# Optimization experiments

Hardware: AMD Instinct MI355X
Metric: run time of the kernel (lower is better)

## Reference

```python
import jax, jax.numpy as jnp
import numpy as np

N, MAX_NB, H, L, V, B, M = 16384, 15, 512, 128, 1024, 256, 65536


def setup_inputs() -> dict:
    key = jax.random.key(0)
    ks = jax.random.split(key, 32)
    s = 0.02  # param init scale
    inp = {
        'x_ids': jax.random.randint(ks[0], (N,), 0, V, dtype=jnp.int32),
        'contexts': jax.random.randint(ks[1], (N,), 0, B, dtype=jnp.int32),
        'nei_idx': jax.random.randint(ks[2], (N, MAX_NB), 0, M, dtype=jnp.int32),
        'nei_mask': jax.random.randint(ks[3], (N, MAX_NB), 0, 2, dtype=jnp.int32),
        'o_idx': jax.random.randint(ks[4], (N, MAX_NB), 0, M, dtype=jnp.int32),
        'o_mask': jax.random.randint(ks[5], (N, MAX_NB), 0, 2, dtype=jnp.int32),
        'H_msg': jax.random.normal(ks[6], (M, H), jnp.float32),
        'x_tree_vecs': jax.random.normal(ks[7], (B, L), jnp.float32),
        'embedding': jax.random.normal(ks[8], (V, H), jnp.float32) * s,
        'Wz_w': jax.random.normal(ks[9], (H, 2 * H), jnp.float32) * s,
        'Wz_b': jnp.zeros((H,), jnp.float32),
        'Wr_w': jax.random.normal(ks[10], (H, H), jnp.float32) * s,
        'Wr_b': jnp.zeros((H,), jnp.float32),
        'Ur_w': jax.random.normal(ks[11], (H, H), jnp.float32) * s,
        'Wh_w': jax.random.normal(ks[12], (H, 2 * H), jnp.float32) * s,
        'Wh_b': jnp.zeros((H,), jnp.float32),
        'W_w': jax.random.normal(ks[13], (H, H + L), jnp.float32) * s,
        'W_b': jnp.zeros((H,), jnp.float32),
        'Wo_w': jax.random.normal(ks[14], (V, H), jnp.float32) * s,
        'Wo_b': jnp.zeros((V,), jnp.float32),
        'Ui_w': jax.random.normal(ks[15], (H, 2 * H), jnp.float32) * s,
        'Ui_b': jnp.zeros((H,), jnp.float32),
        'U_w': jax.random.normal(ks[16], (H, H + L), jnp.float32) * s,
        'U_b': jnp.zeros((H,), jnp.float32),
        'Uo_w': jax.random.normal(ks[17], (1, H), jnp.float32) * s,
        'Uo_b': jnp.zeros((1,), jnp.float32),
    }
    return inp


def _gru(x, h_nei, Wz_w, Wz_b, Wr_w, Wr_b, Ur_w, Wh_w, Wh_b):
    # x: [N,H], h_nei: [N,MAX_NB,H]
    sum_h = h_nei.sum(axis=1)
    z = jax.nn.sigmoid(jnp.concatenate([x, sum_h], axis=1) @ Wz_w.T + Wz_b)
    r1 = (x @ Wr_w.T + Wr_b)[:, None, :]          # [N,1,H]
    r2 = jnp.einsum('nkh,gh->nkg', h_nei, Ur_w)   # U_r(h_nei), no bias
    r = jax.nn.sigmoid(r1 + r2)
    sum_gated = (r * h_nei).sum(axis=1)
    pre_h = jnp.tanh(jnp.concatenate([x, sum_gated], axis=1) @ Wh_w.T + Wh_b)
    return (1.0 - z) * sum_h + z * pre_h


def reference(x_ids, contexts, nei_idx, nei_mask, o_idx, o_mask, H_msg,
              x_tree_vecs, embedding, Wz_w, Wz_b, Wr_w, Wr_b, Ur_w,
              Wh_w, Wh_b, W_w, W_b, Wo_w, Wo_b, Ui_w, Ui_b, U_w, U_b,
              Uo_w, Uo_b):
    x = embedding[x_ids]                                   # [N,H]
    h_nei = H_msg[nei_idx] * nei_mask[..., None].astype(H_msg.dtype)  # [N,NB,H]
    o_nei = H_msg[o_idx] * o_mask[..., None].astype(H_msg.dtype)
    new_h = _gru(x, h_nei, Wz_w, Wz_b, Wr_w, Wr_b, Ur_w, Wh_w, Wh_b)
    cur_o = o_nei.sum(axis=1)                              # [N,H]
    ctx = x_tree_vecs[contexts]                            # [N,L]
    # word prediction: aggregate(new_h, contexts, x_tree_vecs, 'word')
    w_hid = jax.nn.relu(jnp.concatenate([new_h, ctx], axis=1) @ W_w.T + W_b)
    word_scores = w_hid @ Wo_w.T + Wo_b                    # [N,V]
    # stop prediction: U_i(cat(x, cur_o)) -> aggregate(..., 'stop')
    stop_h = jax.nn.relu(jnp.concatenate([x, cur_o], axis=1) @ Ui_w.T + Ui_b)
    s_hid = jax.nn.relu(jnp.concatenate([stop_h, ctx], axis=1) @ U_w.T + U_b)
    stop_scores = s_hid @ Uo_w.T + Uo_b                    # [N,1]
    return jnp.concatenate([word_scores, stop_scores], axis=1)  # [N,V+1]
```

## Files before the change

kernel.cpp:

```cpp
#include <hip/hip_runtime.h>
#include <hip/hip_bf16.h>

typedef unsigned short u16;
typedef unsigned int u32;
typedef __attribute__((ext_vector_type(8))) short s8v;
typedef __attribute__((ext_vector_type(4))) float f4v;

#define HDIM 512
#define NNODE 16384
#define NB 15

__device__ __forceinline__ u16 f2bu(float x) {
  union { float f; u32 i; } v; v.f = x;
  u32 r = v.i + 0x7FFFu + ((v.i >> 16) & 1u);
  return (u16)(r >> 16);
}
__device__ __forceinline__ float bu2f(u16 u) {
  union { u32 i; float f; } v; v.i = ((u32)u) << 16;
  return v.f;
}
__device__ __forceinline__ u32 pk(float a, float b) {
  return (u32)f2bu(a) | ((u32)f2bu(b) << 16);
}
__device__ __forceinline__ float sigm(float x) {
  return __builtin_amdgcn_rcpf(1.f + __expf(-x));
}
__device__ __forceinline__ void gl16(const void* g, void* l) {
  __builtin_amdgcn_global_load_lds(
      (const __attribute__((address_space(1))) u32*)g,
      (__attribute__((address_space(3))) u32*)l, 16, 0, 0);
}

__global__ __launch_bounds__(256) void k_cvt_all(
    const float* Wz_w, const float* Wr_w, const float* Wh_w, const float* Ui_w,
    const float* Ur_w, const float* W_w, const float* U_w, const float* Wo_w,
    const float* emb, const float* xtree,
    const float* Wz_b, const float* Wr_b, const float* Wh_b, const float* Ui_b,
    const float* W_b, const float* U_b,
    u16* wcat, u16* wz_h, u16* wh_h, u16* ui_h, u16* ur, u16* w_n, u16* u_n,
    u16* ccat, u16* wo, u16* emb_bf, u16* xt_bf, float* ebias, float* cbias) {
  int seg = blockIdx.y;
  const float* src = nullptr; u16* dst = nullptr;
  const float* fsrc = nullptr; float* fdst = nullptr;
  int R = 0, Cs = 0, c0 = 0, C = 0, fn = 0;
  switch (seg) {
    case 0:  src = Wz_w; dst = wcat;              R = 512;  Cs = 1024; c0 = 0;   C = 512; break;
    case 1:  src = Wr_w; dst = wcat + 512 * 512;  R = 512;  Cs = 512;  c0 = 0;   C = 512; break;
    case 2:  src = Wh_w; dst = wcat + 1024 * 512; R = 512;  Cs = 1024; c0 = 0;   C = 512; break;
    case 3:  src = Ui_w; dst = wcat + 1536 * 512; R = 512;  Cs = 1024; c0 = 0;   C = 512; break;
    case 4:  src = Wz_w; dst = wz_h;              R = 512;  Cs = 1024; c0 = 512; C = 512; break;
    case 5:  src = Wh_w; dst = wh_h;              R = 512;  Cs = 1024; c0 = 512; C = 512; break;
    case 6:  src = Ui_w; dst = ui_h;              R = 512;  Cs = 1024; c0 = 512; C = 512; break;
    case 7:  src = Ur_w; dst = ur;                R = 512;  Cs = 512;  c0 = 0;   C = 512; break;
    case 8:  src = W_w;  dst = w_n;               R = 512;  Cs = 640;  c0 = 0;   C = 512; break;
    case 9:  src = U_w;  dst = u_n;               R = 512;  Cs = 640;  c0 = 0;   C = 512; break;
    case 10: src = W_w;  dst = ccat;              R = 512;  Cs = 640;  c0 = 512; C = 128; break;
    case 11: src = U_w;  dst = ccat + 512 * 128;  R = 512;  Cs = 640;  c0 = 512; C = 128; break;
    case 12: src = Wo_w; dst = wo;                R = 1024; Cs = 512;  c0 = 0;   C = 512; break;
    case 13: src = emb;  dst = emb_bf;            R = 1024; Cs = 512;  c0 = 0;   C = 512; break;
    case 14: src = xtree; dst = xt_bf;            R = 256;  Cs = 128;  c0 = 0;   C = 128; break;
    case 15: fsrc = Wz_b; fdst = ebias;        fn = 512; break;
    case 16: fsrc = Wr_b; fdst = ebias + 512;  fn = 512; break;
    case 17: fsrc = Wh_b; fdst = ebias + 1024; fn = 512; break;
    case 18: fsrc = Ui_b; fdst = ebias + 1536; fn = 512; break;
    case 19: fsrc = W_b;  fdst = cbias;        fn = 512; break;
    case 20: fsrc = U_b;  fdst = cbias + 512;  fn = 512; break;
  }
  int i = blockIdx.x * 256 + threadIdx.x;
  if (fdst) { if (i < fn) fdst[i] = fsrc[i]; return; }
  int e0 = i * 8;
  if (e0 >= R * C) return;
  int r = e0 / C, c = e0 - r * C;
  const float* s = src + (size_t)r * Cs + c0 + c;
  float4 a = *reinterpret_cast<const float4*>(s);
  float4 b = *reinterpret_cast<const float4*>(s + 4);
  uint4 o = {pk(a.x, a.y), pk(a.z, a.w), pk(b.x, b.y), pk(b.z, b.w)};
  *reinterpret_cast<uint4*>(&dst[e0]) = o;
}

__global__ void k_cvt8(const float* __restrict__ src, u16* __restrict__ dst) {
  size_t i = ((size_t)blockIdx.x * 256 + threadIdx.x) * 8;
  float4 a = *reinterpret_cast<const float4*>(src + i);
  float4 b = *reinterpret_cast<const float4*>(src + i + 4);
  uint4 o = {pk(a.x, a.y), pk(a.z, a.w), pk(b.x, b.y), pk(b.z, b.w)};
  *reinterpret_cast<uint4*>(dst + i) = o;
}

struct GP {
  const u16* A; const u16* B; int K;
  const float* gadd; int ldg; const int* gidx;
  const float* bias; const float* zf; const u16* shb;
  float* outf; u16* outh; int ldo;
};

template<int EP>
__device__ __forceinline__ void epi(int row, int col, float v, const GP& g) {
  if constexpr (EP == 0) {
    g.outf[(size_t)row * g.ldo + col] = v + (g.bias ? g.bias[col] : 0.f);
  } else if constexpr (EP == 1) {
    float pre = v + g.gadd[(size_t)g.gidx[row] * g.ldg + col];
    g.outf[(size_t)row * g.ldo + col] = sigm(pre);
  } else if constexpr (EP == 2) {
    float pre = tanhf(v + g.gadd[(size_t)g.gidx[row] * g.ldg + col]);
    float z = g.zf[(size_t)row * HDIM + col];
    float sh = bu2f(g.shb[(size_t)row * HDIM + col]);
    g.outh[(size_t)row * g.ldo + col] = f2bu((1.f - z) * sh + z * pre);
  } else if constexpr (EP == 3) {
    float pre = v + g.gadd[(size_t)g.gidx[row] * g.ldg + col];
    g.outh[(size_t)row * g.ldo + col] = f2bu(pre > 0.f ? pre : 0.f);
  } else {
    g.outh[(size_t)row * g.ldo + col] = f2bu(v);
  }
}

template<int EP>
__device__ void gemm_core(const GP& g, u16* AsB, u16* BsB) {
  const int tid = threadIdx.x, lane = tid & 63, w = tid >> 6;
  const int wm = (w >> 2) * 64, wn = (w & 3) * 32;
  const int n0 = blockIdx.x * 128, m0 = blockIdx.y * 128;
  const int K = g.K;

  const u16* gA[2]; const u16* gB[2]; int ls[2];
#pragma unroll
  for (int i = 0; i < 2; i++) {
    int slot = tid + i * 512;
    int r = slot >> 3, c = (slot & 7) ^ (r & 7);
    gA[i] = g.A + (size_t)(m0 + r) * K + c * 8;
    gB[i] = g.B + (size_t)(n0 + r) * K + c * 8;
    ls[i] = slot * 8;
  }

  f4v acc[4][2];
  f4v z4 = {0.f, 0.f, 0.f, 0.f};
#pragma unroll
  for (int a = 0; a < 4; a++) { acc[a][0] = z4; acc[a][1] = z4; }

  const int T = K >> 6;
#pragma unroll
  for (int i = 0; i < 2; i++) gl16(gA[i], AsB + ls[i]);
#pragma unroll
  for (int i = 0; i < 2; i++) gl16(gB[i], BsB + ls[i]);

  int cur = 0;
  for (int t = 0; t < T; t++) {
    __syncthreads();
    if (t + 1 < T) {
      int k0 = (t + 1) * 64;
      u16* as = AsB + (cur ^ 1) * 8192;
      u16* bs = BsB + (cur ^ 1) * 8192;
#pragma unroll
      for (int i = 0; i < 2; i++) gl16(gA[i] + k0, as + ls[i]);
#pragma unroll
      for (int i = 0; i < 2; i++) gl16(gB[i] + k0, bs + ls[i]);
    }
    const u16* as = AsB + cur * 8192;
    const u16* bs = BsB + cur * 8192;
#pragma unroll
    for (int ks = 0; ks < 2; ks++) {
      s8v af[4], bf[2];
      int cc = ks * 4 + (lane >> 4);
#pragma unroll
      for (int i = 0; i < 4; i++) {
        int R = wm + i * 16 + (lane & 15);
        af[i] = *reinterpret_cast<const s8v*>(&as[R * 64 + (cc ^ (R & 7)) * 8]);
      }
#pragma unroll
      for (int i = 0; i < 2; i++) {
        int C = wn + i * 16 + (lane & 15);
        bf[i] = *reinterpret_cast<const s8v*>(&bs[C * 64 + (cc ^ (C & 7)) * 8]);
      }
#pragma unroll
      for (int mi = 0; mi < 4; mi++)
#pragma unroll
        for (int ni = 0; ni < 2; ni++)
          acc[mi][ni] = __builtin_amdgcn_mfma_f32_16x16x32_bf16(
              af[mi], bf[ni], acc[mi][ni], 0, 0, 0);
    }
    cur ^= 1;
  }
#pragma unroll
  for (int mi = 0; mi < 4; mi++)
#pragma unroll
    for (int ni = 0; ni < 2; ni++)
#pragma unroll
      for (int r = 0; r < 4; r++) {
        int row = m0 + wm + mi * 16 + (lane >> 4) * 4 + r;
        int col = n0 + wn + ni * 16 + (lane & 15);
        epi<EP>(row, col, acc[mi][ni][r], g);
      }
}

template<int EP>
__global__ __launch_bounds__(512, 4) void k_gemm(GP g) {
  __shared__ u16 As[2 * 128 * 64], Bs[2 * 128 * 64];
  gemm_core<EP>(g, As, Bs);
}

template<int EPa, int EPb>
__global__ __launch_bounds__(512, 4) void k_pair(GP a, GP b) {
  __shared__ u16 As[2 * 128 * 64], Bs[2 * 128 * 64];
  if (blockIdx.z == 0) gemm_core<EPa>(a, As, Bs);
  else gemm_core<EPb>(b, As, Bs);
}

__global__ __launch_bounds__(256) void k_gsr(
    const u16* __restrict__ Hb, const u16* __restrict__ R2,
    const float* __restrict__ E_r, int ldg, const int* __restrict__ x_ids,
    const int* __restrict__ nei_idx, const int* __restrict__ nei_mask,
    const int* __restrict__ o_idx, const int* __restrict__ o_mask,
    u16* __restrict__ sum_h_bf, u16* __restrict__ sg_bf,
    u16* __restrict__ cur_o_bf) {
  int n = blockIdx.x;
  int t = threadIdx.x;
  __shared__ int sidx[NB], smsk[NB], soid[NB], somk[NB];
  __shared__ int sx;
  if (t < NB) {
    sidx[t] = nei_idx[(size_t)n * NB + t];
    smsk[t] = nei_mask[(size_t)n * NB + t];
  } else if (t >= 64 && t < 64 + NB) {
    int k = t - 64;
    soid[k] = o_idx[(size_t)n * NB + k];
    somk[k] = o_mask[(size_t)n * NB + k];
  } else if (t == 128) {
    sx = x_ids[n];
  }
  __syncthreads();
  int c = t * 2;
  const float2 e = *reinterpret_cast<const float2*>(E_r + (size_t)sx * ldg + c);
  float s0 = 0.f, s1 = 0.f, g0 = 0.f, g1 = 0.f, o0 = 0.f, o1 = 0.f;
#pragma unroll
  for (int k = 0; k < NB; k++) {
    if (smsk[k]) {
      u32 hv = *reinterpret_cast<const u32*>(Hb + (size_t)sidx[k] * HDIM + c);
      u32 rv = *reinterpret_cast<const u32*>(R2 + (size_t)sidx[k] * HDIM + c);
      float h0 = bu2f((u16)hv), h1 = bu2f((u16)(hv >> 16));
      float r0 = sigm(bu2f((u16)rv) + e.x);
      float r1 = sigm(bu2f((u16)(rv >> 16)) + e.y);
      s0 += h0; s1 += h1;
      g0 += r0 * h0; g1 += r1 * h1;
    }
    if (somk[k]) {
      u32 v = *reinterpret_cast<const u32*>(Hb + (size_t)soid[k] * HDIM + c);
      o0 += bu2f((u16)v); o1 += bu2f((u16)(v >> 16));
    }
  }
  size_t b = (size_t)n * HDIM + c;
  *reinterpret_cast<u32*>(&sum_h_bf[b]) = pk(s0, s1);
  *reinterpret_cast<u32*>(&sg_bf[b]) = pk(g0, g1);
  *reinterpret_cast<u32*>(&cur_o_bf[b]) = pk(o0, o1);
}

__global__ __launch_bounds__(256) void k_stop(
    const u16* __restrict__ shid, const float* __restrict__ Uo_w,
    const float* __restrict__ Uo_b, float* __restrict__ out) {
  int n = blockIdx.x * 4 + (threadIdx.x >> 6);
  int lane = threadIdx.x & 63;
  float s = 0.f;
  for (int j = lane; j < HDIM; j += 64)
    s += bu2f(shid[(size_t)n * HDIM + j]) * Uo_w[j];
#pragma unroll
  for (int off = 32; off; off >>= 1) s += __shfl_xor(s, off, 64);
  if (lane == 0) out[(size_t)n * 1025 + 1024] = s + Uo_b[0];
}

extern "C" void kernel_launch(void* const* d_in, const int* in_sizes, int n_in,
                              void* d_out, int out_size, void* d_ws, size_t ws_size,
                              hipStream_t stream) {
  const int* x_ids = (const int*)d_in[0];
  const int* contexts = (const int*)d_in[1];
  const int* nei_idx = (const int*)d_in[2];
  const int* nei_mask = (const int*)d_in[3];
  const int* o_idx = (const int*)d_in[4];
  const int* o_mask = (const int*)d_in[5];
  const float* H_msg = (const float*)d_in[6];
  const float* xtree = (const float*)d_in[7];
  const float* emb = (const float*)d_in[8];
  const float* Wz_w = (const float*)d_in[9];  const float* Wz_b = (const float*)d_in[10];
  const float* Wr_w = (const float*)d_in[11]; const float* Wr_b = (const float*)d_in[12];
  const float* Ur_w = (const float*)d_in[13];
  const float* Wh_w = (const float*)d_in[14]; const float* Wh_b = (const float*)d_in[15];
  const float* W_w  = (const float*)d_in[16]; const float* W_b  = (const float*)d_in[17];
  const float* Wo_w = (const float*)d_in[18]; const float* Wo_b = (const float*)d_in[19];
  const float* Ui_w = (const float*)d_in[20]; const float* Ui_b = (const float*)d_in[21];
  const float* U_w  = (const float*)d_in[22]; const float* U_b  = (const float*)d_in[23];
  const float* Uo_w = (const float*)d_in[24]; const float* Uo_b = (const float*)d_in[25];
  float* out = (float*)d_out;
  const int M = 65536;

  char* base = (char*)d_ws;
  size_t ofs = 0;
  auto alloc = [&](size_t bytes) -> char* {
    char* p = base + ofs;
    ofs = (ofs + bytes + 255) & ~(size_t)255;
    return p;
  };
  u16* wcat  = (u16*)alloc((size_t)2048 * 512 * 2);
  u16* wz_h  = (u16*)alloc(512 * 512 * 2);
  u16* wh_h  = (u16*)alloc(512 * 512 * 2);
  u16* ui_h  = (u16*)alloc(512 * 512 * 2);
  u16* ur    = (u16*)alloc(512 * 512 * 2);
  u16* w_n   = (u16*)alloc(512 * 512 * 2);
  u16* u_n   = (u16*)alloc(512 * 512 * 2);
  u16* ccat  = (u16*)alloc(1024 * 128 * 2);
  u16* wo    = (u16*)alloc(1024 * 512 * 2);
  u16* emb_bf = (u16*)alloc(1024 * 512 * 2);
  u16* xt_bf  = (u16*)alloc(256 * 128 * 2);
  float* ebias = (float*)alloc(2048 * 4);
  float* cbias = (float*)alloc(1024 * 4);
  float* E_cat = (float*)alloc((size_t)1024 * 2048 * 4);
  float* C_cat = (float*)alloc((size_t)256 * 1024 * 4);
  u16* H_bf = (u16*)alloc((size_t)M * HDIM * 2);
  u16* R2   = (u16*)alloc((size_t)M * HDIM * 2);
  float* z_f = (float*)alloc((size_t)NNODE * HDIM * 4);
  u16* sum_h_bf = (u16*)alloc((size_t)NNODE * HDIM * 2);
  u16* cur_o_bf = (u16*)alloc((size_t)NNODE * HDIM * 2);
  u16* sg_bf    = (u16*)alloc((size_t)NNODE * HDIM * 2);
  u16* newh_bf  = (u16*)alloc((size_t)NNODE * HDIM * 2);
  u16* whid_bf  = (u16*)alloc((size_t)NNODE * HDIM * 2);
  u16* stoph_bf = (u16*)alloc((size_t)NNODE * HDIM * 2);
  u16* shid_bf  = (u16*)alloc((size_t)NNODE * HDIM * 2);

  k_cvt_all<<<dim3(256, 21), dim3(256), 0, stream>>>(
      Wz_w, Wr_w, Wh_w, Ui_w, Ur_w, W_w, U_w, Wo_w, emb, xtree,
      Wz_b, Wr_b, Wh_b, Ui_b, W_b, U_b,
      wcat, wz_h, wh_h, ui_h, ur, w_n, u_n, ccat, wo, emb_bf, xt_bf,
      ebias, cbias);
  k_cvt8<<<dim3(16384), dim3(256), 0, stream>>>(H_msg, H_bf);

  GP ge{emb_bf, wcat, 512, nullptr, 0, nullptr, ebias, nullptr, nullptr,
        E_cat, nullptr, 2048};
  k_gemm<0><<<dim3(16, 8), dim3(512), 0, stream>>>(ge);
  GP gc{xt_bf, ccat, 128, nullptr, 0, nullptr, cbias, nullptr, nullptr,
        C_cat, nullptr, 1024};
  k_gemm<0><<<dim3(8, 2), dim3(512), 0, stream>>>(gc);

  GP gr{H_bf, ur, 512, nullptr, 0, nullptr, nullptr, nullptr, nullptr,
        nullptr, R2, 512};
  k_gemm<4><<<dim3(4, 512), dim3(512), 0, stream>>>(gr);

  k_gsr<<<dim3(NNODE), dim3(256), 0, stream>>>(
      H_bf, R2, E_cat + 512, 2048, x_ids, nei_idx, nei_mask, o_idx, o_mask,
      sum_h_bf, sg_bf, cur_o_bf);

  GP gz{sum_h_bf, wz_h, 512, E_cat, 2048, x_ids, nullptr, nullptr, nullptr,
        z_f, nullptr, 512};
  GP gs{cur_o_bf, ui_h, 512, E_cat + 1536, 2048, x_ids, nullptr, nullptr, nullptr,
        nullptr, stoph_bf, 512};
  k_pair<1, 3><<<dim3(4, 128, 2), dim3(512), 0, stream>>>(gz, gs);

  GP gn{sg_bf, wh_h, 512, E_cat + 1024, 2048, x_ids, nullptr, z_f, sum_h_bf,
        nullptr, newh_bf, 512};
  k_gemm<2><<<dim3(4, 128), dim3(512), 0, stream>>>(gn);

  GP gw{newh_bf, w_n, 512, C_cat, 1024, contexts, nullptr, nullptr, nullptr,
        nullptr, whid_bf, 512};
  GP gu{stoph_bf, u_n, 512, C_cat + 512, 1024, contexts, nullptr, nullptr, nullptr,
        nullptr, shid_bf, 512};
  k_pair<3, 3><<<dim3(4, 128, 2), dim3(512), 0, stream>>>(gw, gu);

  GP gword{whid_bf, wo, 512, nullptr, 0, nullptr, Wo_b, nullptr, nullptr,
           out, nullptr, 1025};
  k_gemm<0><<<dim3(8, 128), dim3(512), 0, stream>>>(gword);

  k_stop<<<dim3(NNODE / 4), dim3(256), 0, stream>>>(shid_bf, Uo_w, Uo_b, out);
}
```

Baseline: 358.0 us.

## Fuse z and candidate GEMMs, interleave H and R2 rows, swizzle tile order

The z-gate GEMM and the candidate-state GEMM now run in one kernel with two accumulator sets. That kernel computes sigmoid, tanh and the GRU blend in its epilogue, so the fp32 z buffer and its round trip through memory go away. H_bf and R2 are stored interleaved in a single [M,1024] buffer, so each gathered neighbor row brings H and R from adjacent memory. GEMM tiles are also remapped with a stride-8 swizzle to change L2 locality across blocks. The costs are higher register pressure in the fused kernel, which has no double buffering, and the stop GEMM now launches alone instead of paired.

Result: faster. 333.0 us (-7.0%).

```diff
diff --git a/kernel.cpp b/kernel.cpp
--- a/kernel.cpp
+++ b/kernel.cpp
@@ -78,18 +78,19 @@
   *reinterpret_cast<uint4*>(&dst[e0]) = o;
 }
 
-__global__ void k_cvt8(const float* __restrict__ src, u16* __restrict__ dst) {
+__global__ void k_cvtH(const float* __restrict__ src, u16* __restrict__ HR) {
   size_t i = ((size_t)blockIdx.x * 256 + threadIdx.x) * 8;
+  size_t m = i >> 9, c = i & 511;
   float4 a = *reinterpret_cast<const float4*>(src + i);
   float4 b = *reinterpret_cast<const float4*>(src + i + 4);
   uint4 o = {pk(a.x, a.y), pk(a.z, a.w), pk(b.x, b.y), pk(b.z, b.w)};
-  *reinterpret_cast<uint4*>(dst + i) = o;
+  *reinterpret_cast<uint4*>(&HR[m * 1024 + c]) = o;
 }
 
 struct GP {
-  const u16* A; const u16* B; int K;
+  const u16* A; const u16* B; int K; int lda;
   const float* gadd; int ldg; const int* gidx;
-  const float* bias; const float* zf; const u16* shb;
+  const float* bias; const u16* shb;
   float* outf; u16* outh; int ldo;
 };
 
@@ -97,14 +98,6 @@
 __device__ __forceinline__ void epi(int row, int col, float v, const GP& g) {
   if constexpr (EP == 0) {
     g.outf[(size_t)row * g.ldo + col] = v + (g.bias ? g.bias[col] : 0.f);
-  } else if constexpr (EP == 1) {
-    float pre = v + g.gadd[(size_t)g.gidx[row] * g.ldg + col];
-    g.outf[(size_t)row * g.ldo + col] = sigm(pre);
-  } else if constexpr (EP == 2) {
-    float pre = tanhf(v + g.gadd[(size_t)g.gidx[row] * g.ldg + col]);
-    float z = g.zf[(size_t)row * HDIM + col];
-    float sh = bu2f(g.shb[(size_t)row * HDIM + col]);
-    g.outh[(size_t)row * g.ldo + col] = f2bu((1.f - z) * sh + z * pre);
   } else if constexpr (EP == 3) {
     float pre = v + g.gadd[(size_t)g.gidx[row] * g.ldg + col];
     g.outh[(size_t)row * g.ldo + col] = f2bu(pre > 0.f ? pre : 0.f);
@@ -117,7 +110,11 @@
 __device__ void gemm_core(const GP& g, u16* AsB, u16* BsB) {
   const int tid = threadIdx.x, lane = tid & 63, w = tid >> 6;
   const int wm = (w >> 2) * 64, wn = (w & 3) * 32;
-  const int n0 = blockIdx.x * 128, m0 = blockIdx.y * 128;
+  const int nx = gridDim.x;
+  int orig = blockIdx.y * nx + blockIdx.x;
+  int q = (nx * gridDim.y) >> 3;
+  int tile = (orig & 7) * q + (orig >> 3);
+  const int n0 = (tile % nx) * 128, m0 = (tile / nx) * 128;
   const int K = g.K;
 
   const u16* gA[2]; const u16* gB[2]; int ls[2];
@@ -125,7 +122,7 @@
   for (int i = 0; i < 2; i++) {
     int slot = tid + i * 512;
     int r = slot >> 3, c = (slot & 7) ^ (r & 7);
-    gA[i] = g.A + (size_t)(m0 + r) * K + c * 8;
+    gA[i] = g.A + (size_t)(m0 + r) * g.lda + c * 8;
     gB[i] = g.B + (size_t)(n0 + r) * K + c * 8;
     ls[i] = slot * 8;
   }
@@ -203,8 +200,114 @@
   else gemm_core<EPb>(b, As, Bs);
 }
 
+__global__ __launch_bounds__(512, 4) void k_zn(
+    const u16* __restrict__ sumh, const u16* __restrict__ sg,
+    const u16* __restrict__ Wz, const u16* __restrict__ Wh,
+    const float* __restrict__ E_z, const float* __restrict__ E_h, int ldg,
+    const int* __restrict__ gidx, u16* __restrict__ newh) {
+  __shared__ u16 As1[128 * 64], Bs1[128 * 64], As2[128 * 64], Bs2[128 * 64];
+  const int tid = threadIdx.x, lane = tid & 63, w = tid >> 6;
+  const int wm = (w >> 2) * 64, wn = (w & 3) * 32;
+  const int nx = gridDim.x;
+  int orig = blockIdx.y * nx + blockIdx.x;
+  int q = (nx * gridDim.y) >> 3;
+  int tile = (orig & 7) * q + (orig >> 3);
+  const int n0 = (tile % nx) * 128, m0 = (tile / nx) * 128;
+
+  const u16 *gA1[2], *gA2[2], *gB1[2], *gB2[2]; int ls[2];
+#pragma unroll
+  for (int i = 0; i < 2; i++) {
+    int slot = tid + i * 512;
+    int r = slot >> 3, c = (slot & 7) ^ (r & 7);
+    gA1[i] = sumh + (size_t)(m0 + r) * HDIM + c * 8;
+    gA2[i] = sg + (size_t)(m0 + r) * HDIM + c * 8;
+    gB1[i] = Wz + (size_t)(n0 + r) * HDIM + c * 8;
+    gB2[i] = Wh + (size_t)(n0 + r) * HDIM + c * 8;
+    ls[i] = slot * 8;
+  }
+
+  f4v az[4][2], ah[4][2];
+  f4v z4 = {0.f, 0.f, 0.f, 0.f};
+#pragma unroll
+  for (int a = 0; a < 4; a++) {
+    az[a][0] = z4; az[a][1] = z4; ah[a][0] = z4; ah[a][1] = z4;
+  }
+
+  for (int k0 = 0; k0 < HDIM; k0 += 64) {
+    __syncthreads();
+#pragma unroll
+    for (int i = 0; i < 2; i++) gl16(gA1[i] + k0, As1 + ls[i]);
+#pragma unroll
+    for (int i = 0; i < 2; i++) gl16(gB1[i] + k0, Bs1 + ls[i]);
+#pragma unroll
+    for (int i = 0; i < 2; i++) gl16(gA2[i] + k0, As2 + ls[i]);
+#pragma unroll
+    for (int i = 0; i < 2; i++) gl16(gB2[i] + k0, Bs2 + ls[i]);
+    __syncthreads();
+#pragma unroll
+    for (int ks = 0; ks < 2; ks++) {
+      int cc = ks * 4 + (lane >> 4);
+      {
+        s8v af[4], bf[2];
+#pragma unroll
+        for (int i = 0; i < 4; i++) {
+          int R = wm + i * 16 + (lane & 15);
+          af[i] = *reinterpret_cast<const s8v*>(&As1[R * 64 + (cc ^ (R & 7)) * 8]);
+        }
+#pragma unroll
+        for (int i = 0; i < 2; i++) {
+          int C = wn + i * 16 + (lane & 15);
+          bf[i] = *reinterpret_cast<const s8v*>(&Bs1[C * 64 + (cc ^ (C & 7)) * 8]);
+        }
+#pragma unroll
+        for (int mi = 0; mi < 4; mi++)
+#pragma unroll
+          for (int ni = 0; ni < 2; ni++)
+            az[mi][ni] = __builtin_amdgcn_mfma_f32_16x16x32_bf16(
+                af[mi], bf[ni], az[mi][ni], 0, 0, 0);
+      }
+      {
+        s8v af[4], bf[2];
+#pragma unroll
+        for (int i = 0; i < 4; i++) {
+          int R = wm + i * 16 + (lane & 15);
+          af[i] = *reinterpret_cast<const s8v*>(&As2[R * 64 + (cc ^ (R & 7)) * 8]);
+        }
+#pragma unroll
+        for (int i = 0; i < 2; i++) {
+          int C = wn + i * 16 + (lane & 15);
+          bf[i] = *reinterpret_cast<const s8v*>(&Bs2[C * 64 + (cc ^ (C & 7)) * 8]);
+        }
+#pragma unroll
+        for (int mi = 0; mi < 4; mi++)
+#pragma unroll
+          for (int ni = 0; ni < 2; ni++)
+            ah[mi][ni] = __builtin_amdgcn_mfma_f32_16x16x32_bf16(
+                af[mi], bf[ni], ah[mi][ni], 0, 0, 0);
+      }
+    }
+  }
+#pragma unroll
+  for (int mi = 0; mi < 4; mi++)
+#pragma unroll
+    for (int r = 0; r < 4; r++) {
+      int row = m0 + wm + mi * 16 + (lane >> 4) * 4 + r;
+      int xid = gidx[row];
+      const float* ez = E_z + (size_t)xid * ldg;
+      const float* eh = E_h + (size_t)xid * ldg;
+#pragma unroll
+      for (int ni = 0; ni < 2; ni++) {
+        int col = n0 + wn + ni * 16 + (lane & 15);
+        float zv = sigm(az[mi][ni][r] + ez[col]);
+        float pre = tanhf(ah[mi][ni][r] + eh[col]);
+        float sh = bu2f(sumh[(size_t)row * HDIM + col]);
+        newh[(size_t)row * HDIM + col] = f2bu((1.f - zv) * sh + zv * pre);
+      }
+    }
+}
+
 __global__ __launch_bounds__(256) void k_gsr(
-    const u16* __restrict__ Hb, const u16* __restrict__ R2,
+    const u16* __restrict__ HR,
     const float* __restrict__ E_r, int ldg, const int* __restrict__ x_ids,
     const int* __restrict__ nei_idx, const int* __restrict__ nei_mask,
     const int* __restrict__ o_idx, const int* __restrict__ o_mask,
@@ -231,8 +334,9 @@
 #pragma unroll
   for (int k = 0; k < NB; k++) {
     if (smsk[k]) {
-      u32 hv = *reinterpret_cast<const u32*>(Hb + (size_t)sidx[k] * HDIM + c);
-      u32 rv = *reinterpret_cast<const u32*>(R2 + (size_t)sidx[k] * HDIM + c);
+      const u16* row = HR + (size_t)sidx[k] * 1024;
+      u32 hv = *reinterpret_cast<const u32*>(row + c);
+      u32 rv = *reinterpret_cast<const u32*>(row + 512 + c);
       float h0 = bu2f((u16)hv), h1 = bu2f((u16)(hv >> 16));
       float r0 = sigm(bu2f((u16)rv) + e.x);
       float r1 = sigm(bu2f((u16)(rv >> 16)) + e.y);
@@ -240,7 +344,7 @@
       g0 += r0 * h0; g1 += r1 * h1;
     }
     if (somk[k]) {
-      u32 v = *reinterpret_cast<const u32*>(Hb + (size_t)soid[k] * HDIM + c);
+      u32 v = *reinterpret_cast<const u32*>(HR + (size_t)soid[k] * 1024 + c);
       o0 += bu2f((u16)v); o1 += bu2f((u16)(v >> 16));
     }
   }
@@ -309,9 +413,7 @@
   float* cbias = (float*)alloc(1024 * 4);
   float* E_cat = (float*)alloc((size_t)1024 * 2048 * 4);
   float* C_cat = (float*)alloc((size_t)256 * 1024 * 4);
-  u16* H_bf = (u16*)alloc((size_t)M * HDIM * 2);
-  u16* R2   = (u16*)alloc((size_t)M * HDIM * 2);
-  float* z_f = (float*)alloc((size_t)NNODE * HDIM * 4);
+  u16* HR = (u16*)alloc((size_t)M * 1024 * 2);
   u16* sum_h_bf = (u16*)alloc((size_t)NNODE * HDIM * 2);
   u16* cur_o_bf = (u16*)alloc((size_t)NNODE * HDIM * 2);
   u16* sg_bf    = (u16*)alloc((size_t)NNODE * HDIM * 2);
@@ -325,40 +427,37 @@
       Wz_b, Wr_b, Wh_b, Ui_b, W_b, U_b,
       wcat, wz_h, wh_h, ui_h, ur, w_n, u_n, ccat, wo, emb_bf, xt_bf,
       ebias, cbias);
-  k_cvt8<<<dim3(16384), dim3(256), 0, stream>>>(H_msg, H_bf);
-
-  GP ge{emb_bf, wcat, 512, nullptr, 0, nullptr, ebias, nullptr, nullptr,
+  k_cvtH<<<dim3(16384), dim3(256), 0, stream>>>(H_msg, HR);
+
+  GP ge{emb_bf, wcat, 512, 512, nullptr, 0, nullptr, ebias, nullptr,
         E_cat, nullptr, 2048};
   k_gemm<0><<<dim3(16, 8), dim3(512), 0, stream>>>(ge);
-  GP gc{xt_bf, ccat, 128, nullptr, 0, nullptr, cbias, nullptr, nullptr,
+  GP gc{xt_bf, ccat, 128, 128, nullptr, 0, nullptr, cbias, nullptr,
         C_cat, nullptr, 1024};
   k_gemm<0><<<dim3(8, 2), dim3(512), 0, stream>>>(gc);
 
-  GP gr{H_bf, ur, 512, nullptr, 0, nullptr, nullptr, nullptr, nullptr,
-        nullptr, R2, 512};
+  GP gr{HR, ur, 512, 1024, nullptr, 0, nullptr, nullptr, nullptr,
+        nullptr, HR + 512, 1024};
   k_gemm<4><<<dim3(4, 512), dim3(512), 0, stream>>>(gr);
 
   k_gsr<<<dim3(NNODE), dim3(256), 0, stream>>>(
-      H_bf, R2, E_cat + 512, 2048, x_ids, nei_idx, nei_mask, o_idx, o_mask,
+      HR, E_cat + 512, 2048, x_ids, nei_idx, nei_mask, o_idx, o_mask,
       sum_h_bf, sg_bf, cur_o_bf);
 
-  GP gz{sum_h_bf, wz_h, 512, E_cat, 2048, x_ids, nullptr, nullptr, nullptr,
-        z_f, nullptr, 512};
-  GP gs{cur_o_bf, ui_h, 512, E_cat + 1536, 2048, x_ids, nullptr, nullptr, nullptr,
+  GP gs{cur_o_bf, ui_h, 512, 512, E_cat + 1536, 2048, x_ids, nullptr, nullptr,
         nullptr, stoph_bf, 512};
-  k_pair<1, 3><<<dim3(4, 128, 2), dim3(512), 0, stream>>>(gz, gs);
-
-  GP gn{sg_bf, wh_h, 512, E_cat + 1024, 2048, x_ids, nullptr, z_f, sum_h_bf,
-        nullptr, newh_bf, 512};
-  k_gemm<2><<<dim3(4, 128), dim3(512), 0, stream>>>(gn);
-
-  GP gw{newh_bf, w_n, 512, C_cat, 1024, contexts, nullptr, nullptr, nullptr,
+  k_gemm<3><<<dim3(4, 128), dim3(512), 0, stream>>>(gs);
+
+  k_zn<<<dim3(4, 128), dim3(512), 0, stream>>>(
+      sum_h_bf, sg_bf, wz_h, wh_h, E_cat, E_cat + 1024, 2048, x_ids, newh_bf);
+
+  GP gw{newh_bf, w_n, 512, 512, C_cat, 1024, contexts, nullptr, nullptr,
         nullptr, whid_bf, 512};
-  GP gu{stoph_bf, u_n, 512, C_cat + 512, 1024, contexts, nullptr, nullptr, nullptr,
+  GP gu{stoph_bf, u_n, 512, 512, C_cat + 512, 1024, contexts, nullptr, nullptr,
         nullptr, shid_bf, 512};
   k_pair<3, 3><<<dim3(4, 128, 2), dim3(512), 0, stream>>>(gw, gu);
 
-  GP gword{whid_bf, wo, 512, nullptr, 0, nullptr, Wo_b, nullptr, nullptr,
+  GP gword{whid_bf, wo, 512, 512, nullptr, 0, nullptr, Wo_b, nullptr,
            out, nullptr, 1025};
   k_gemm<0><<<dim3(8, 128), dim3(512), 0, stream>>>(gword);
 
```
